# Performance work log

Measured on AMD Instinct MI355X. Metric: run time of the kernel, lower is better.

The kernel has to match this reference:

```python
import jax, jax.numpy as jnp
import numpy as np

B, N, DIM, H, DH = 8, 1024, 512, 8, 64
INNER = H * DH  # 512
G = DH // 4     # SE(3) groups of size 4 per head


def setup_inputs() -> dict:
    key = jax.random.key(0)
    ks = jax.random.split(key, 6)
    x = jax.random.normal(ks[0], (B, N, DIM), jnp.float32)
    rotations = jax.random.normal(ks[1], (B, N, 3, 3), jnp.float32)
    translations = jax.random.normal(ks[2], (B, N, 3), jnp.float32)
    # JaxLinear init: trunc-normal std = 1/sqrt(fan_in), zero bias
    w_qkv = jax.random.normal(ks[3], (DIM, 3 * INNER), jnp.float32) * (1.0 / np.sqrt(DIM))
    b_qkv = jnp.zeros((3 * INNER,), jnp.float32)
    w_out = jax.random.normal(ks[4], (INNER, DIM), jnp.float32) * (1.0 / np.sqrt(INNER))
    b_out = jnp.zeros((DIM,), jnp.float32)
    return {"x": x, "rotations": rotations, "translations": translations,
            "w_qkv": w_qkv, "b_qkv": b_qkv, "w_out": w_out, "b_out": b_out}


def _apply_pose(P, t, transpose):
    # P: [B,N,4,4]; t: [B,H,N,DH] -> reshape to groups of 4 and rotate each group
    tg = t.reshape(B, H, N, G, 4)
    sub = 'bnji,bhncj->bhnci' if transpose else 'bnij,bhncj->bhnci'
    return jnp.einsum(sub, P, tg).reshape(B, H, N, DH)


def reference(x, rotations, translations, w_qkv, b_qkv, w_out, b_out):
    scale = DH ** -0.5
    qkv = x @ w_qkv + b_qkv                      # [B,N,3*INNER]
    q, k, v = jnp.split(qkv, 3, axis=-1)
    to_heads = lambda t: t.reshape(B, N, H, DH).transpose(0, 2, 1, 3)  # b n (h d) -> b h n d
    q, k, v = to_heads(q), to_heads(k), to_heads(v)

    # SE(3) pose matrices
    eye4 = jnp.eye(4, dtype=x.dtype)
    Rt = jnp.swapaxes(rotations, -1, -2)
    t_inv = -jnp.einsum('bnij,bnj->bni', Rt, translations)
    P_qinv = (jnp.broadcast_to(eye4, (B, N, 4, 4))
              .at[..., :3, :3].set(Rt)
              .at[..., :3, 3].set(t_inv))       # inverted query poses
    P_kv = (jnp.broadcast_to(eye4, (B, N, 4, 4))
            .at[..., :3, :3].set(rotations)
            .at[..., :3, 3].set(translations))  # key/value poses

    # per-token rotation of q/k/v (q uses P_qinv^T per original einsum)
    q = _apply_pose(P_qinv, q, transpose=True)
    k = _apply_pose(P_kv, k, transpose=False)
    v = _apply_pose(P_kv, v, transpose=False)   # v_transform=True

    attn = jax.nn.softmax(jnp.einsum('bhqd,bhkd->bhqk', q, k) * scale, axis=-1)
    out = jnp.einsum('bhqk,bhkd->bhqd', attn, v)
    out = _apply_pose(P_qinv, out, transpose=False)  # inverse transform on output

    out = out.transpose(0, 2, 1, 3).reshape(B, N, INNER)  # b h n d -> b n (h d)
    return out @ w_out + b_out
```

## Files before the change

### kernel.cpp

```cpp
#include <hip/hip_runtime.h>
#include <math.h>

#define BSZ   8
#define NSEQ  1024
#define DIM   512
#define NH    8
#define DH    64
#define INNER 512
#define NTOK  (BSZ*NSEQ)
#define QKVN  (3*INNER)

typedef __bf16   bf16x8 __attribute__((ext_vector_type(8)));
typedef _Float16 f16x8  __attribute__((ext_vector_type(8)));
typedef float    f32x4  __attribute__((ext_vector_type(4)));

#define QSCL (0.125f * 1.44269504088896f)

#define ATTN_P_OFF 49152
#define ATTN_LDS   67584

static __device__ __forceinline__ ushort f2bf(float f) {
    union { float f; unsigned u; } v; v.f = f;
    unsigned r = (v.u + 0x7FFFu + ((v.u >> 16) & 1u)) >> 16;
    return (ushort)r;
}
static __device__ __forceinline__ ushort f2h(float f) {
    _Float16 h = (_Float16)f;
    return __builtin_bit_cast(unsigned short, h);
}
static __device__ __forceinline__ void async16(const void* g, void* l) {
    __builtin_amdgcn_global_load_lds(
        (const __attribute__((address_space(1))) unsigned int*)g,
        (__attribute__((address_space(3))) unsigned int*)l, 16, 0, 0);
}

__global__ __launch_bounds__(256) void prep_kernel(
    const float* __restrict__ x,  ushort* __restrict__ xf,
    const float* __restrict__ wq, ushort* __restrict__ wqT,
    const float* __restrict__ wo, ushort* __restrict__ woT)
{
    const int bid = blockIdx.x;
    if (bid < 4096) {
        const int i = bid*256 + threadIdx.x;
        float4 v = ((const float4*)x)[i];
        ushort4 h = { f2h(v.x), f2h(v.y), f2h(v.z), f2h(v.w) };
        ((ushort4*)xf)[i] = h;
        return;
    }
    __shared__ float tile[32][33];
    int K, F, bx, by; const float* in; ushort* outp; int is_q;
    if (bid < 4096 + 768) {
        const int id = bid - 4096;
        bx = id % 48; by = id / 48;
        K = DIM; F = QKVN; in = wq; outp = wqT; is_q = 1;
    } else {
        const int id = bid - 4864;
        bx = id % 16; by = id / 16;
        K = INNER; F = DIM; in = wo; outp = woT; is_q = 0;
    }
    const int lx = threadIdx.x & 31, ly = threadIdx.x >> 5;
#pragma unroll
    for (int u = 0; u < 4; u++) {
        const int k = by*32 + ly + u*8;
        tile[ly + u*8][lx] = in[(size_t)k*F + bx*32 + lx];
    }
    __syncthreads();
#pragma unroll
    for (int u = 0; u < 4; u++) {
        const int f = bx*32 + ly + u*8;
        const float v = tile[lx][ly + u*8];
        outp[(size_t)f*K + by*32 + lx] = is_q ? f2h(v) : f2bf(v);
    }
}

__global__ __launch_bounds__(256) void qkv_gemm_f16(
    const ushort* __restrict__ Ag,
    const ushort* __restrict__ Bg,
    const float* __restrict__ bias, const float* __restrict__ rot,
    const float* __restrict__ trans,
    ushort* __restrict__ qb, ushort* __restrict__ kb, ushort* __restrict__ vt)
{
    extern __shared__ __align__(16) char smem[];

    const int tid  = threadIdx.x;
    const int lane = tid & 63;
    const int w    = tid >> 6;
    const int c    = lane & 15;
    const int quad = lane >> 4;
    const int wr   = w >> 1, wc = w & 1;
    const int tn   = blockIdx.x;
    const int tf   = blockIdx.y;

    f32x4 acc[4][4] = {};

    const int part = w >> 1;
    const int g0   = (w & 1) * 4;
    const ushort* src = (part == 0) ? Ag : Bg;
    const ushort* wbase = src + (size_t)((part == 0 ? tf : tn)*128 + g0*16 + c)*DIM
                          + quad*8;

    auto stage = [&](int k0, int buf) {
#pragma unroll
        for (int g = 0; g < 4; g++)
            async16(wbase + (size_t)g*16*DIM + k0,
                    smem + buf*16384 + part*8192 + (g0 + g)*1024);
    };

    stage(0, 0);

    for (int ch = 0; ch < 16; ch++) {
        const int cur = ch & 1, nxt = cur ^ 1;
        if (ch < 15) {
            stage((ch+1)*32, nxt);
            __asm__ volatile("s_waitcnt vmcnt(4)\n\ts_barrier" ::: "memory");
        } else {
            __asm__ volatile("s_waitcnt vmcnt(0)\n\ts_barrier" ::: "memory");
        }

        const char* B = smem + cur*16384;
        f16x8 fa[4], fb[4];
#pragma unroll
        for (int i = 0; i < 4; i++)
            fa[i] = *(const f16x8*)(B + (wr*4 + i)*1024 + lane*16);
#pragma unroll
        for (int j = 0; j < 4; j++)
            fb[j] = *(const f16x8*)(B + 8192 + (wc*4 + j)*1024 + lane*16);
#pragma unroll
        for (int i = 0; i < 4; i++)
#pragma unroll
            for (int j = 0; j < 4; j++)
                acc[i][j] = __builtin_amdgcn_mfma_f32_16x16x32_f16(
                    fa[i], fb[j], acc[i][j], 0, 0, 0);
        __asm__ volatile("s_waitcnt lgkmcnt(0)\n\ts_barrier" ::: "memory");
    }

    const int sec = tf >> 2;

#pragma unroll
    for (int j = 0; j < 4; j++) {
        const int tc = tn*128 + wc*64 + j*16 + c;
        const int bb = tc >> 10, n = tc & 1023;
        const float* R = rot   + (size_t)(bb*NSEQ + n)*9;
        const float* T = trans + (size_t)(bb*NSEQ + n)*3;
        const float R0=R[0],R1=R[1],R2=R[2],R3=R[3],R4=R[4],R5=R[5],R6=R[6],R7=R[7],R8=R[8];
        const float T0=T[0],T1=T[1],T2=T[2];
        float ti0 = 0.f, ti1 = 0.f, ti2 = 0.f;
        if (sec == 0) {
            ti0 = -(R0*T0 + R3*T1 + R6*T2);
            ti1 = -(R1*T0 + R4*T1 + R7*T2);
            ti2 = -(R2*T0 + R5*T1 + R8*T2);
        }
#pragma unroll
        for (int i = 0; i < 4; i++) {
            const int fr = tf*128 + wr*64 + i*16 + quad*4;
            const int fl = fr & 511;
            const int h  = fl >> 6, d = fl & 63;
            float4 bv = *(const float4*)(bias + fr);
            const float g0v = acc[i][j][0] + bv.x;
            const float g1v = acc[i][j][1] + bv.y;
            const float g2v = acc[i][j][2] + bv.z;
            const float g3v = acc[i][j][3] + bv.w;
            if (sec == 0) {
                float o0 = (R0*g0v + R1*g1v + R2*g2v) * QSCL;
                float o1 = (R3*g0v + R4*g1v + R5*g2v) * QSCL;
                float o2 = (R6*g0v + R7*g1v + R8*g2v) * QSCL;
                float o3 = (ti0*g0v + ti1*g1v + ti2*g2v + g3v) * QSCL;
                ushort4 ov = { f2bf(o0), f2bf(o1), f2bf(o2), f2bf(o3) };
                *(ushort4*)(qb + ((size_t)((bb*NH + h)*NSEQ + n))*DH + d) = ov;
            } else {
                float o0 = R0*g0v + R1*g1v + R2*g2v + T0*g3v;
                float o1 = R3*g0v + R4*g1v + R5*g2v + T1*g3v;
                float o2 = R6*g0v + R7*g1v + R8*g2v + T2*g3v;
                float o3 = g3v;
                if (sec == 1) {
                    ushort4 ov = { f2bf(o0), f2bf(o1), f2bf(o2), f2bf(o3) };
                    *(ushort4*)(kb + ((size_t)((bb*NH + h)*NSEQ + n))*DH + d) = ov;
                } else {
                    ushort* vtb = vt + ((size_t)(bb*NH + h)*DH + d)*NSEQ + n;
                    vtb[0*NSEQ] = f2bf(o0);
                    vtb[1*NSEQ] = f2bf(o1);
                    vtb[2*NSEQ] = f2bf(o2);
                    vtb[3*NSEQ] = f2bf(o3);
                }
            }
        }
    }
}

__global__ __launch_bounds__(256) void attn_mfma_kernel(
    const ushort* __restrict__ qb, const ushort* __restrict__ kb,
    const ushort* __restrict__ vt, const float* __restrict__ rot,
    const float* __restrict__ trans, ushort* __restrict__ om)
{
    extern __shared__ __align__(16) char smem[];

    const int tid  = threadIdx.x;
    const int lane = tid & 63;
    const int w    = tid >> 6;
    const int c    = lane & 15;
    const int quad = lane >> 4;

    const int qt = blockIdx.x;
    const int bh = blockIdx.y;
    const int bb = bh >> 3, h = bh & 7;

    const ushort* Q = qb + (size_t)bh * NSEQ * DH;
    const ushort* K = kb + (size_t)bh * NSEQ * DH;
    const ushort* V = vt + (size_t)bh * DH * NSEQ;

    bf16x8 qf[2][2];
#pragma unroll
    for (int m = 0; m < 2; m++) {
        const ushort* qrow = Q + (size_t)(qt*128 + w*32 + m*16 + c)*DH + quad*8;
        qf[m][0] = *(const bf16x8*)(qrow);
        qf[m][1] = *(const bf16x8*)(qrow + 32);
    }

    f32x4 Oacc[2][4] = {};
    float lsum[2][4] = {};

    auto stage = [&](int kt, int buf) {
#pragma unroll
        for (int u = 0; u < 2; u++) {
            const int seg = w + u*4;
            const int nt = seg >> 1, hh = seg & 1;
            const ushort* g = K + (size_t)(kt*64 + nt*16 + c)*DH + hh*32 + quad*8;
            async16(g, smem + buf*16384 + seg*1024);
        }
#pragma unroll
        for (int u = 0; u < 2; u++) {
            const int s2 = w + u*4;
            const int nt = s2 >> 1, kc = s2 & 1;
            const ushort* g = V + (size_t)(nt*16 + c)*NSEQ + kt*64 + kc*32 + quad*8;
            async16(g, smem + buf*16384 + 8192 + s2*1024);
        }
    };

    stage(0, 0);
    stage(1, 1);

    for (int kt = 0; kt < 16; kt++) {
        const int cur = kt % 3;
        if (kt < 15) {
            __asm__ volatile("s_waitcnt vmcnt(4)\n\ts_barrier" ::: "memory");
        } else {
            __asm__ volatile("s_waitcnt vmcnt(0)\n\ts_barrier" ::: "memory");
        }
        if (kt < 14) stage(kt + 2, (kt + 2) % 3);

        const char* Kb = smem + cur*16384;
        const char* Vb = smem + cur*16384 + 8192;

        f32x4 s[2][4];
#pragma unroll
        for (int nt = 0; nt < 4; nt++) {
            bf16x8 k0 = *(const bf16x8*)(Kb + (nt*2+0)*1024 + lane*16);
            bf16x8 k1 = *(const bf16x8*)(Kb + (nt*2+1)*1024 + lane*16);
#pragma unroll
            for (int m = 0; m < 2; m++) {
                f32x4 a = {0.f, 0.f, 0.f, 0.f};
                a = __builtin_amdgcn_mfma_f32_16x16x32_bf16(qf[m][0], k0, a, 0, 0, 0);
                a = __builtin_amdgcn_mfma_f32_16x16x32_bf16(qf[m][1], k1, a, 0, 0, 0);
                s[m][nt] = a;
            }
        }

#pragma unroll
        for (int m = 0; m < 2; m++) {
            ushort (*Psw)[72] = (ushort (*)[72])(smem + ATTN_P_OFF + (w*2+m)*2304);
#pragma unroll
            for (int nt = 0; nt < 4; nt++)
#pragma unroll
                for (int r = 0; r < 4; r++) {
                    const float p = exp2f(s[m][nt][r]);
                    lsum[m][r] += p;
                    Psw[quad*4 + r][nt*16 + c] = (ushort)__builtin_bit_cast(
                        unsigned short, (__bf16)p);
                }
        }
        __asm__ volatile("s_waitcnt lgkmcnt(0)" ::: "memory");

#pragma unroll
        for (int kc = 0; kc < 2; kc++) {
            bf16x8 vfr[4];
#pragma unroll
            for (int nt = 0; nt < 4; nt++)
                vfr[nt] = *(const bf16x8*)(Vb + (nt*2+kc)*1024 + lane*16);
#pragma unroll
            for (int m = 0; m < 2; m++) {
                ushort (*Psw)[72] = (ushort (*)[72])(smem + ATTN_P_OFF + (w*2+m)*2304);
                bf16x8 a = *(const bf16x8*)&Psw[c][kc*32 + quad*8];
#pragma unroll
                for (int nt = 0; nt < 4; nt++)
                    Oacc[m][nt] = __builtin_amdgcn_mfma_f32_16x16x32_bf16(
                        a, vfr[nt], Oacc[m][nt], 0, 0, 0);
            }
        }
    }

#pragma unroll
    for (int mk = 1; mk < 16; mk <<= 1)
#pragma unroll
        for (int m = 0; m < 2; m++)
#pragma unroll
            for (int r = 0; r < 4; r++)
                lsum[m][r] += __shfl_xor(lsum[m][r], mk);

    __syncthreads();
    float (*Osh)[68] = (float (*)[68])smem;
    {
        float inv[2][4];
#pragma unroll
        for (int m = 0; m < 2; m++)
#pragma unroll
            for (int r = 0; r < 4; r++) inv[m][r] = 1.f / lsum[m][r];
#pragma unroll
        for (int m = 0; m < 2; m++)
#pragma unroll
            for (int nt = 0; nt < 4; nt++)
#pragma unroll
                for (int r = 0; r < 4; r++)
                    Osh[w*32 + m*16 + quad*4 + r][nt*16 + c] =
                        Oacc[m][nt][r] * inv[m][r];
    }
    __syncthreads();

#pragma unroll
    for (int u = 0; u < 8; u++) {
        const int t   = tid + u*256;
        const int row = t >> 4;
        const int g   = t & 15;
        const int n   = qt*128 + row;
        const float o0 = Osh[row][g*4+0], o1 = Osh[row][g*4+1];
        const float o2 = Osh[row][g*4+2], o3 = Osh[row][g*4+3];
        const float* R = rot   + (size_t)(bb*NSEQ + n)*9;
        const float* T = trans + (size_t)(bb*NSEQ + n)*3;
        const float ti0 = -(R[0]*T[0] + R[3]*T[1] + R[6]*T[2]);
        const float ti1 = -(R[1]*T[0] + R[4]*T[1] + R[7]*T[2]);
        const float ti2 = -(R[2]*T[0] + R[5]*T[1] + R[8]*T[2]);
        const float p0 = R[0]*o0 + R[3]*o1 + R[6]*o2 + ti0*o3;
        const float p1 = R[1]*o0 + R[4]*o1 + R[7]*o2 + ti1*o3;
        const float p2 = R[2]*o0 + R[5]*o1 + R[8]*o2 + ti2*o3;
        const float p3 = o3;
        ushort4 hv = { f2bf(p0), f2bf(p1), f2bf(p2), f2bf(p3) };
        *(ushort4*)(om + (size_t)(bb*NSEQ + n)*INNER + h*DH + g*4) = hv;
    }
}

__global__ __launch_bounds__(256) void out_gemm_mfma(
    const ushort* __restrict__ Ag, const ushort* __restrict__ Bg,
    const float* __restrict__ bias, float* __restrict__ out)
{
    extern __shared__ __align__(16) char smem[];

    const int tid  = threadIdx.x;
    const int lane = tid & 63;
    const int w    = tid >> 6;
    const int c    = lane & 15;
    const int quad = lane >> 4;
    const int wr   = w >> 1, wc = w & 1;
    const int tn   = blockIdx.x;
    const int tf   = blockIdx.y;

    f32x4 acc[4][4] = {};

    const int part = w >> 1;
    const int g0   = (w & 1) * 4;
    const ushort* src = (part == 0) ? Ag : Bg;
    const ushort* wbase = src + (size_t)((part == 0 ? tf : tn)*128 + g0*16 + c)*INNER
                          + quad*8;

    auto stage = [&](int k0, int buf) {
#pragma unroll
        for (int g = 0; g < 4; g++)
            async16(wbase + (size_t)g*16*INNER + k0,
                    smem + buf*16384 + part*8192 + (g0 + g)*1024);
    };

    stage(0, 0);
    stage(32, 1);
    stage(64, 2);

    for (int ch = 0; ch < 16; ch++) {
        const int cur = ch & 3;
        if (ch < 14) {
            __asm__ volatile("s_waitcnt vmcnt(8)\n\ts_barrier" ::: "memory");
        } else if (ch == 14) {
            __asm__ volatile("s_waitcnt vmcnt(4)\n\ts_barrier" ::: "memory");
        } else {
            __asm__ volatile("s_waitcnt vmcnt(0)\n\ts_barrier" ::: "memory");
        }
        if (ch < 13) stage((ch+3)*32, (ch+3) & 3);

        const char* B = smem + cur*16384;
        bf16x8 fa[4], fb[4];
#pragma unroll
        for (int i = 0; i < 4; i++)
            fa[i] = *(const bf16x8*)(B + (wr*4 + i)*1024 + lane*16);
#pragma unroll
        for (int j = 0; j < 4; j++)
            fb[j] = *(const bf16x8*)(B + 8192 + (wc*4 + j)*1024 + lane*16);
#pragma unroll
        for (int i = 0; i < 4; i++)
#pragma unroll
            for (int j = 0; j < 4; j++)
                acc[i][j] = __builtin_amdgcn_mfma_f32_16x16x32_bf16(
                    fa[i], fb[j], acc[i][j], 0, 0, 0);
    }

#pragma unroll
    for (int j = 0; j < 4; j++) {
        const int tc = tn*128 + wc*64 + j*16 + c;
#pragma unroll
        for (int i = 0; i < 4; i++) {
            const int fr = tf*128 + wr*64 + i*16 + quad*4;
            float4 bv = *(const float4*)(bias + fr);
            float4 ov = { acc[i][j][0] + bv.x, acc[i][j][1] + bv.y,
                          acc[i][j][2] + bv.z, acc[i][j][3] + bv.w };
            *(float4*)(out + (size_t)tc*DIM + fr) = ov;
        }
    }
}

extern "C" void kernel_launch(void* const* d_in, const int* in_sizes, int n_in,
                              void* d_out, int out_size, void* d_ws, size_t ws_size,
                              hipStream_t stream) {
    (void)in_sizes; (void)n_in; (void)out_size; (void)ws_size;
    const float* x     = (const float*)d_in[0];
    const float* rot   = (const float*)d_in[1];
    const float* trans = (const float*)d_in[2];
    const float* w_qkv = (const float*)d_in[3];
    const float* b_qkv = (const float*)d_in[4];
    const float* w_out = (const float*)d_in[5];
    const float* b_out = (const float*)d_in[6];
    float* out = (float*)d_out;

    const size_t HB = (size_t)BSZ*NH*NSEQ*DH;
    ushort* qb   = (ushort*)d_ws;
    ushort* kb   = qb   + HB;
    ushort* vt   = kb   + HB;
    ushort* woTh = vt   + HB;
    ushort* wqTh = woTh + (size_t)DIM*INNER;
    ushort* xf   = wqTh + (size_t)QKVN*DIM;
    ushort* om   = xf;

    static int s_attr_done = 0;
    if (!s_attr_done) {
        (void)hipFuncSetAttribute((const void*)attn_mfma_kernel,
            hipFuncAttributeMaxDynamicSharedMemorySize, ATTN_LDS);
        (void)hipFuncSetAttribute((const void*)out_gemm_mfma,
            hipFuncAttributeMaxDynamicSharedMemorySize, 65536);
        s_attr_done = 1;
    }

    prep_kernel<<<dim3(5120), 256, 0, stream>>>(
        x, xf, w_qkv, wqTh, w_out, woTh);

    qkv_gemm_f16<<<dim3(NTOK/128, QKVN/128), 256, 32768, stream>>>(
        wqTh, xf, b_qkv, rot, trans, qb, kb, vt);
    attn_mfma_kernel<<<dim3(NSEQ/128, BSZ*NH), 256, ATTN_LDS, stream>>>(
        qb, kb, vt, rot, trans, om);
    out_gemm_mfma<<<dim3(NTOK/128, DIM/128), 256, 65536, stream>>>(
        woTh, om, b_out, out);
}
```

Measured before the change: 164.7 us.

## Load K/V fragments directly from global memory and remap attention blocks for locality

Drops the triple-buffered async LDS staging of K and V tiles in the attention kernel. Each wave now reads its MFMA fragments straight from global memory, relying on L2/cache reuse across the four waves, and block-level barriers are removed. LDS shrinks to a static 34 KB buffer holding only the P scratch, which may allow more resident blocks per CU. The grid is also flattened to 1D with a swizzled block index, so consecutive blocks map to different batch-heads. The risk is redundant global traffic and more exposed load latency, since there is no longer explicit prefetch overlap.

```diff
diff --git a/kernel.cpp b/kernel.cpp
--- a/kernel.cpp
+++ b/kernel.cpp
@@ -15,9 +15,6 @@
 typedef float    f32x4  __attribute__((ext_vector_type(4)));
 
 #define QSCL (0.125f * 1.44269504088896f)
-
-#define ATTN_P_OFF 49152
-#define ATTN_LDS   67584
 
 static __device__ __forceinline__ ushort f2bf(float f) {
     union { float f; unsigned u; } v; v.f = f;
@@ -192,7 +189,7 @@
     const ushort* __restrict__ vt, const float* __restrict__ rot,
     const float* __restrict__ trans, ushort* __restrict__ om)
 {
-    extern __shared__ __align__(16) char smem[];
+    __shared__ __align__(16) char smem[34816];
 
     const int tid  = threadIdx.x;
     const int lane = tid & 63;
@@ -200,8 +197,10 @@
     const int c    = lane & 15;
     const int quad = lane >> 4;
 
-    const int qt = blockIdx.x;
-    const int bh = blockIdx.y;
+    const int o   = blockIdx.x;
+    const int wid = (o & 7) * 64 + (o >> 3);
+    const int qt  = wid & 7;
+    const int bh  = wid >> 3;
     const int bb = bh >> 3, h = bh & 7;
 
     const ushort* Q = qb + (size_t)bh * NSEQ * DH;
@@ -219,43 +218,13 @@
     f32x4 Oacc[2][4] = {};
     float lsum[2][4] = {};
 
-    auto stage = [&](int kt, int buf) {
-#pragma unroll
-        for (int u = 0; u < 2; u++) {
-            const int seg = w + u*4;
-            const int nt = seg >> 1, hh = seg & 1;
-            const ushort* g = K + (size_t)(kt*64 + nt*16 + c)*DH + hh*32 + quad*8;
-            async16(g, smem + buf*16384 + seg*1024);
-        }
-#pragma unroll
-        for (int u = 0; u < 2; u++) {
-            const int s2 = w + u*4;
-            const int nt = s2 >> 1, kc = s2 & 1;
-            const ushort* g = V + (size_t)(nt*16 + c)*NSEQ + kt*64 + kc*32 + quad*8;
-            async16(g, smem + buf*16384 + 8192 + s2*1024);
-        }
-    };
-
-    stage(0, 0);
-    stage(1, 1);
-
     for (int kt = 0; kt < 16; kt++) {
-        const int cur = kt % 3;
-        if (kt < 15) {
-            __asm__ volatile("s_waitcnt vmcnt(4)\n\ts_barrier" ::: "memory");
-        } else {
-            __asm__ volatile("s_waitcnt vmcnt(0)\n\ts_barrier" ::: "memory");
-        }
-        if (kt < 14) stage(kt + 2, (kt + 2) % 3);
-
-        const char* Kb = smem + cur*16384;
-        const char* Vb = smem + cur*16384 + 8192;
-
         f32x4 s[2][4];
 #pragma unroll
         for (int nt = 0; nt < 4; nt++) {
-            bf16x8 k0 = *(const bf16x8*)(Kb + (nt*2+0)*1024 + lane*16);
-            bf16x8 k1 = *(const bf16x8*)(Kb + (nt*2+1)*1024 + lane*16);
+            const ushort* kr = K + (size_t)(kt*64 + nt*16 + c)*DH + quad*8;
+            bf16x8 k0 = *(const bf16x8*)(kr);
+            bf16x8 k1 = *(const bf16x8*)(kr + 32);
 #pragma unroll
             for (int m = 0; m < 2; m++) {
                 f32x4 a = {0.f, 0.f, 0.f, 0.f};
@@ -265,9 +234,17 @@
             }
         }
 
+        bf16x8 vfr[2][4];
+#pragma unroll
+        for (int kc = 0; kc < 2; kc++)
+#pragma unroll
+            for (int nt = 0; nt < 4; nt++)
+                vfr[kc][nt] = *(const bf16x8*)(
+                    V + (size_t)(nt*16 + c)*NSEQ + kt*64 + kc*32 + quad*8);
+
 #pragma unroll
         for (int m = 0; m < 2; m++) {
-            ushort (*Psw)[72] = (ushort (*)[72])(smem + ATTN_P_OFF + (w*2+m)*2304);
+            ushort (*Psw)[72] = (ushort (*)[72])(smem + (w*2+m)*2304);
 #pragma unroll
             for (int nt = 0; nt < 4; nt++)
 #pragma unroll
@@ -282,18 +259,14 @@
 
 #pragma unroll
         for (int kc = 0; kc < 2; kc++) {
-            bf16x8 vfr[4];
-#pragma unroll
-            for (int nt = 0; nt < 4; nt++)
-                vfr[nt] = *(const bf16x8*)(Vb + (nt*2+kc)*1024 + lane*16);
 #pragma unroll
             for (int m = 0; m < 2; m++) {
-                ushort (*Psw)[72] = (ushort (*)[72])(smem + ATTN_P_OFF + (w*2+m)*2304);
+                ushort (*Psw)[72] = (ushort (*)[72])(smem + (w*2+m)*2304);
                 bf16x8 a = *(const bf16x8*)&Psw[c][kc*32 + quad*8];
 #pragma unroll
                 for (int nt = 0; nt < 4; nt++)
                     Oacc[m][nt] = __builtin_amdgcn_mfma_f32_16x16x32_bf16(
-                        a, vfr[nt], Oacc[m][nt], 0, 0, 0);
+                        a, vfr[kc][nt], Oacc[m][nt], 0, 0, 0);
             }
         }
     }
@@ -446,8 +419,6 @@
 
     static int s_attr_done = 0;
     if (!s_attr_done) {
-        (void)hipFuncSetAttribute((const void*)attn_mfma_kernel,
-            hipFuncAttributeMaxDynamicSharedMemorySize, ATTN_LDS);
         (void)hipFuncSetAttribute((const void*)out_gemm_mfma,
             hipFuncAttributeMaxDynamicSharedMemorySize, 65536);
         s_attr_done = 1;
@@ -458,7 +429,7 @@
 
     qkv_gemm_f16<<<dim3(NTOK/128, QKVN/128), 256, 32768, stream>>>(
         wqTh, xf, b_qkv, rot, trans, qb, kb, vt);
-    attn_mfma_kernel<<<dim3(NSEQ/128, BSZ*NH), 256, ATTN_LDS, stream>>>(
+    attn_mfma_kernel<<<dim3(512), 256, 0, stream>>>(
         qb, kb, vt, rot, trans, om);
     out_gemm_mfma<<<dim3(NTOK/128, DIM/128), 256, 65536, stream>>>(
         woTh, om, b_out, out);
```

New measurement: 190.6 us. 15.7% more time.

## Shrink attention query tile to 64 rows with double-buffered static LDS

Applied to the files above, without the earlier changes.

The attention kernel now processes 64 query rows per block (16 per wave) instead of 128. It replaces the triple-buffered dynamic LDS with a smaller double-buffered static array and adds a launch bound targeting three blocks per CU. The grid becomes 1D with a swizzled mapping so consecutive blocks are spread across batch-head pairs. This doubles the block count to fill the 256 CUs better and raises occupancy. In exchange, K/V tiles are reloaded twice as often per query row, and an extra barrier each iteration plus shallower prefetch depth may expose load latency.

```diff
diff --git a/kernel.cpp b/kernel.cpp
--- a/kernel.cpp
+++ b/kernel.cpp
@@ -15,9 +15,6 @@
 typedef float    f32x4  __attribute__((ext_vector_type(4)));
 
 #define QSCL (0.125f * 1.44269504088896f)
-
-#define ATTN_P_OFF 49152
-#define ATTN_LDS   67584
 
 static __device__ __forceinline__ ushort f2bf(float f) {
     union { float f; unsigned u; } v; v.f = f;
@@ -187,12 +184,12 @@
     }
 }
 
-__global__ __launch_bounds__(256) void attn_mfma_kernel(
+__global__ __launch_bounds__(256, 3) void attn_mfma_kernel(
     const ushort* __restrict__ qb, const ushort* __restrict__ kb,
     const ushort* __restrict__ vt, const float* __restrict__ rot,
     const float* __restrict__ trans, ushort* __restrict__ om)
 {
-    extern __shared__ __align__(16) char smem[];
+    __shared__ __align__(16) char smem[41984];
 
     const int tid  = threadIdx.x;
     const int lane = tid & 63;
@@ -200,24 +197,25 @@
     const int c    = lane & 15;
     const int quad = lane >> 4;
 
-    const int qt = blockIdx.x;
-    const int bh = blockIdx.y;
+    const int o   = blockIdx.x;
+    const int wid = (o & 7) * 128 + (o >> 3);
+    const int qt  = wid & 15;
+    const int bh  = wid >> 4;
     const int bb = bh >> 3, h = bh & 7;
 
     const ushort* Q = qb + (size_t)bh * NSEQ * DH;
     const ushort* K = kb + (size_t)bh * NSEQ * DH;
     const ushort* V = vt + (size_t)bh * DH * NSEQ;
 
-    bf16x8 qf[2][2];
-#pragma unroll
-    for (int m = 0; m < 2; m++) {
-        const ushort* qrow = Q + (size_t)(qt*128 + w*32 + m*16 + c)*DH + quad*8;
-        qf[m][0] = *(const bf16x8*)(qrow);
-        qf[m][1] = *(const bf16x8*)(qrow + 32);
-    }
-
-    f32x4 Oacc[2][4] = {};
-    float lsum[2][4] = {};
+    bf16x8 qf[2];
+    {
+        const ushort* qrow = Q + (size_t)(qt*64 + w*16 + c)*DH + quad*8;
+        qf[0] = *(const bf16x8*)(qrow);
+        qf[1] = *(const bf16x8*)(qrow + 32);
+    }
+
+    f32x4 Oacc[4] = {};
+    float lsum[4] = {};
 
     auto stage = [&](int kt, int buf) {
 #pragma unroll
@@ -237,100 +235,84 @@
     };
 
     stage(0, 0);
-    stage(1, 1);
+
+    ushort (*Psw)[72] = (ushort (*)[72])(smem + 32768 + w*2304);
 
     for (int kt = 0; kt < 16; kt++) {
-        const int cur = kt % 3;
+        const int cur = kt & 1, nxt = cur ^ 1;
         if (kt < 15) {
+            stage(kt+1, nxt);
             __asm__ volatile("s_waitcnt vmcnt(4)\n\ts_barrier" ::: "memory");
         } else {
             __asm__ volatile("s_waitcnt vmcnt(0)\n\ts_barrier" ::: "memory");
         }
-        if (kt < 14) stage(kt + 2, (kt + 2) % 3);
 
         const char* Kb = smem + cur*16384;
         const char* Vb = smem + cur*16384 + 8192;
 
-        f32x4 s[2][4];
+        f32x4 s[4];
 #pragma unroll
         for (int nt = 0; nt < 4; nt++) {
             bf16x8 k0 = *(const bf16x8*)(Kb + (nt*2+0)*1024 + lane*16);
             bf16x8 k1 = *(const bf16x8*)(Kb + (nt*2+1)*1024 + lane*16);
-#pragma unroll
-            for (int m = 0; m < 2; m++) {
-                f32x4 a = {0.f, 0.f, 0.f, 0.f};
-                a = __builtin_amdgcn_mfma_f32_16x16x32_bf16(qf[m][0], k0, a, 0, 0, 0);
-                a = __builtin_amdgcn_mfma_f32_16x16x32_bf16(qf[m][1], k1, a, 0, 0, 0);
-                s[m][nt] = a;
+            f32x4 a = {0.f, 0.f, 0.f, 0.f};
+            a = __builtin_amdgcn_mfma_f32_16x16x32_bf16(qf[0], k0, a, 0, 0, 0);
+            a = __builtin_amdgcn_mfma_f32_16x16x32_bf16(qf[1], k1, a, 0, 0, 0);
+            s[nt] = a;
+        }
+
+#pragma unroll
+        for (int nt = 0; nt < 4; nt++)
+#pragma unroll
+            for (int r = 0; r < 4; r++) {
+                const float p = exp2f(s[nt][r]);
+                lsum[r] += p;
+                Psw[quad*4 + r][nt*16 + c] = (ushort)__builtin_bit_cast(
+                    unsigned short, (__bf16)p);
             }
-        }
-
-#pragma unroll
-        for (int m = 0; m < 2; m++) {
-            ushort (*Psw)[72] = (ushort (*)[72])(smem + ATTN_P_OFF + (w*2+m)*2304);
+        __asm__ volatile("s_waitcnt lgkmcnt(0)" ::: "memory");
+
+#pragma unroll
+        for (int kc2 = 0; kc2 < 2; kc2++) {
+            bf16x8 vfr[4];
 #pragma unroll
             for (int nt = 0; nt < 4; nt++)
-#pragma unroll
-                for (int r = 0; r < 4; r++) {
-                    const float p = exp2f(s[m][nt][r]);
-                    lsum[m][r] += p;
-                    Psw[quad*4 + r][nt*16 + c] = (ushort)__builtin_bit_cast(
-                        unsigned short, (__bf16)p);
-                }
-        }
-        __asm__ volatile("s_waitcnt lgkmcnt(0)" ::: "memory");
-
-#pragma unroll
-        for (int kc = 0; kc < 2; kc++) {
-            bf16x8 vfr[4];
+                vfr[nt] = *(const bf16x8*)(Vb + (nt*2+kc2)*1024 + lane*16);
+            bf16x8 a = *(const bf16x8*)&Psw[c][kc2*32 + quad*8];
 #pragma unroll
             for (int nt = 0; nt < 4; nt++)
-                vfr[nt] = *(const bf16x8*)(Vb + (nt*2+kc)*1024 + lane*16);
-#pragma unroll
-            for (int m = 0; m < 2; m++) {
-                ushort (*Psw)[72] = (ushort (*)[72])(smem + ATTN_P_OFF + (w*2+m)*2304);
-                bf16x8 a = *(const bf16x8*)&Psw[c][kc*32 + quad*8];
-#pragma unroll
-                for (int nt = 0; nt < 4; nt++)
-                    Oacc[m][nt] = __builtin_amdgcn_mfma_f32_16x16x32_bf16(
-                        a, vfr[nt], Oacc[m][nt], 0, 0, 0);
-            }
-        }
+                Oacc[nt] = __builtin_amdgcn_mfma_f32_16x16x32_bf16(
+                    a, vfr[nt], Oacc[nt], 0, 0, 0);
+        }
+        __asm__ volatile("s_waitcnt lgkmcnt(0)\n\ts_barrier" ::: "memory");
     }
 
 #pragma unroll
     for (int mk = 1; mk < 16; mk <<= 1)
 #pragma unroll
-        for (int m = 0; m < 2; m++)
-#pragma unroll
-            for (int r = 0; r < 4; r++)
-                lsum[m][r] += __shfl_xor(lsum[m][r], mk);
+        for (int r = 0; r < 4; r++)
+            lsum[r] += __shfl_xor(lsum[r], mk);
 
     __syncthreads();
     float (*Osh)[68] = (float (*)[68])smem;
     {
-        float inv[2][4];
-#pragma unroll
-        for (int m = 0; m < 2; m++)
-#pragma unroll
-            for (int r = 0; r < 4; r++) inv[m][r] = 1.f / lsum[m][r];
-#pragma unroll
-        for (int m = 0; m < 2; m++)
-#pragma unroll
-            for (int nt = 0; nt < 4; nt++)
-#pragma unroll
-                for (int r = 0; r < 4; r++)
-                    Osh[w*32 + m*16 + quad*4 + r][nt*16 + c] =
-                        Oacc[m][nt][r] * inv[m][r];
+        float inv[4];
+#pragma unroll
+        for (int r = 0; r < 4; r++) inv[r] = 1.f / lsum[r];
+#pragma unroll
+        for (int nt = 0; nt < 4; nt++)
+#pragma unroll
+            for (int r = 0; r < 4; r++)
+                Osh[w*16 + quad*4 + r][nt*16 + c] = Oacc[nt][r] * inv[r];
     }
     __syncthreads();
 
 #pragma unroll
-    for (int u = 0; u < 8; u++) {
+    for (int u = 0; u < 4; u++) {
         const int t   = tid + u*256;
         const int row = t >> 4;
         const int g   = t & 15;
-        const int n   = qt*128 + row;
+        const int n   = qt*64 + row;
         const float o0 = Osh[row][g*4+0], o1 = Osh[row][g*4+1];
         const float o2 = Osh[row][g*4+2], o3 = Osh[row][g*4+3];
         const float* R = rot   + (size_t)(bb*NSEQ + n)*9;
@@ -446,8 +428,6 @@
 
     static int s_attr_done = 0;
     if (!s_attr_done) {
-        (void)hipFuncSetAttribute((const void*)attn_mfma_kernel,
-            hipFuncAttributeMaxDynamicSharedMemorySize, ATTN_LDS);
         (void)hipFuncSetAttribute((const void*)out_gemm_mfma,
             hipFuncAttributeMaxDynamicSharedMemorySize, 65536);
         s_attr_done = 1;
@@ -458,7 +438,7 @@
 
     qkv_gemm_f16<<<dim3(NTOK/128, QKVN/128), 256, 32768, stream>>>(
         wqTh, xf, b_qkv, rot, trans, qb, kb, vt);
-    attn_mfma_kernel<<<dim3(NSEQ/128, BSZ*NH), 256, ATTN_LDS, stream>>>(
+    attn_mfma_kernel<<<dim3(1024), 256, 0, stream>>>(
         qb, kb, vt, rot, trans, om);
     out_gemm_mfma<<<dim3(NTOK/128, DIM/128), 256, 65536, stream>>>(
         woTh, om, b_out, out);
```

New measurement: 167.5 us. Within noise of the previous version (+1.7%).
